# Optimization experiments

Measured on AMD Instinct MI355X. Metric: run time of the kernel, lower is better.

Reference implementation:

```python
import jax, jax.numpy as jnp
import numpy as np

B, T_OUT, C, L = 8, 8, 64, 1024  # batch, temporal channels, spatial channels (=in_channels), time steps


def setup_inputs() -> dict:
    key = jax.random.key(0)
    ks = jax.random.split(key, 7)
    s = 1.0 / np.sqrt(C)  # conv1d default init scale
    return {
        "x": jax.random.normal(ks[0], (B, T_OUT, C, L), dtype=jnp.float32),
        "Wq": jax.random.uniform(ks[1], (C, C), jnp.float32, -s, s),
        "bq": jax.random.uniform(ks[2], (C,), jnp.float32, -s, s),
        "Wk": jax.random.uniform(ks[3], (C, C), jnp.float32, -s, s),
        "bk": jax.random.uniform(ks[4], (C,), jnp.float32, -s, s),
        "Wv": jax.random.uniform(ks[5], (C, C), jnp.float32, -s, s),
        "bv": jax.random.uniform(ks[6], (C,), jnp.float32, -s, s),
    }


def reference(x, Wq, bq, Wk, bk, Wv, bv):
    b, t, c, l = x.shape
    xr = x.reshape(b * t, c, l)  # [BT, C, L]
    # 1x1 Conv1d == per-timestep linear over channels
    q = jnp.einsum('oc,bcl->bol', Wq, xr) + bq[:, None]
    k = jnp.einsum('oc,bcl->bol', Wk, xr) + bk[:, None]
    v = jnp.einsum('oc,bcl->bol', Wv, xr) + bv[:, None]
    # scores[b, i, j] = sum_c q[b, c, i] * k[b, c, j]  -> [BT, L, L]
    scores = jnp.einsum('bci,bcj->bij', q, k)
    weights = jax.nn.softmax(scores, axis=-1)
    # out[b, i, c] = sum_j weights[b, i, j] * v[b, c, j]
    out = jnp.einsum('bij,bcj->bic', weights, v)
    out = jnp.transpose(out, (0, 2, 1))  # [BT, C, L]
    return out.reshape(b, t, c, l)
```

## Files before the change

### kernel.cpp

```cpp
#include <hip/hip_runtime.h>
#include <hip/hip_bf16.h>

#define CC 64
#define LL 1024
#define LOG2E 1.44269504f

typedef unsigned short u16;
typedef unsigned int u32;
typedef __attribute__((ext_vector_type(8))) short short8;
typedef __attribute__((ext_vector_type(4))) float floatx4;

static __device__ __forceinline__ u16 f2b(float f) {
  return (u16)((__float_as_uint(f) + 0x8000u) >> 16);
}
static __device__ __forceinline__ u32 pk2(float a, float b) {
  return ((__float_as_uint(a) + 0x8000u) >> 16) |
         ((__float_as_uint(b) + 0x8000u) & 0xffff0000u);
}
static __device__ __forceinline__ u32 pk2t(float a, float b) {
  return __builtin_amdgcn_perm(__float_as_uint(b), __float_as_uint(a), 0x07060302u);
}
static __device__ __forceinline__ short8 mk8(u32 a, u32 b, u32 c, u32 d) {
  union { u32 u[4]; short8 s; } t;
  t.u[0] = a; t.u[1] = b; t.u[2] = c; t.u[3] = d;
  return t.s;
}

__global__ __launch_bounds__(256) void w_prep(
    const float* __restrict__ Wq, const float* __restrict__ bq,
    const float* __restrict__ Wk, const float* __restrict__ bk,
    const float* __restrict__ Wv, const float* __restrict__ bv,
    u16* __restrict__ whi, float* __restrict__ bsc)
{
  const int idx = blockIdx.x * 256 + threadIdx.x;
  const int m = idx >> 12;
  const float* W = (m == 0) ? Wq : (m == 1) ? Wk : Wv;
  const float w = W[idx & 4095] * ((m == 0) ? LOG2E : 1.0f);
  whi[idx] = f2b(w);
  if (blockIdx.x == 0 && threadIdx.x < 192)
    bsc[threadIdx.x] = (threadIdx.x < 64) ? bq[threadIdx.x] * LOG2E
                     : (threadIdx.x < 128) ? bk[threadIdx.x - 64] : bv[threadIdx.x - 128];
}

__global__ __launch_bounds__(256) void qkv_kernel(
    const float* __restrict__ x,
    const u16* __restrict__ whi, const float* __restrict__ bsc,
    u16* __restrict__ qT, u16* __restrict__ kT, u16* __restrict__ vO)
{
  __shared__ __align__(16) u16 xh_s[2][64 * 72];
  __shared__ __align__(16) u16 tbuf[4 * 16 * 72];
  __shared__ float b_s[192];

  const int tid  = threadIdx.x;
  const int wave = tid >> 6;
  const int lane = tid & 63;
  const int l16  = lane & 15;
  const int quad = lane >> 4;

  const int bt = blockIdx.x & 63;
  const int l0 = (blockIdx.x >> 6) << 7;

  const int lx = tid & 63;
  const int cg = (tid >> 6) << 4;
  const float* xp = x + ((size_t)bt * CC + cg) * LL + l0 + lx;

  {
    float v0[16];
    #pragma unroll
    for (int e = 0; e < 16; ++e) v0[e] = xp[(size_t)e * LL];
    #pragma unroll
    for (int e = 0; e < 16; e += 2)
      *(u32*)(&xh_s[0][0] + lx * 72 + cg + e) = pk2(v0[e], v0[e + 1]);
    if (tid < 192) b_s[tid] = bsc[tid];
  }
  __syncthreads();

  float v1[16];
  #pragma unroll
  for (int e = 0; e < 16; ++e) v1[e] = xp[64 + (size_t)e * LL];

  u16* tb = tbuf + wave * (16 * 72);

  auto compute = [&](int ch) {
    const int lc0 = l0 + (ch << 6);
    const u16* xr_h = &xh_s[ch][0] + (wave * 16 + l16) * 72 + quad * 8;
    const short8 xh0 = *(const short8*)(xr_h);
    const short8 xh1 = *(const short8*)(xr_h + 32);

    #pragma unroll
    for (int ot = 0; ot < 12; ++ot) {
      const int m = ot >> 2;
      const int off = (m << 12) + (((ot & 3) * 16 + l16) << 6) + quad * 8;
      const short8 ah0 = *(const short8*)(whi + off);
      const short8 ah1 = *(const short8*)(whi + off + 32);

      floatx4 acc = (floatx4){0.f, 0.f, 0.f, 0.f};
      acc = __builtin_amdgcn_mfma_f32_16x16x32_bf16(ah0, xh0, acc, 0, 0, 0);
      acc = __builtin_amdgcn_mfma_f32_16x16x32_bf16(ah1, xh1, acc, 0, 0, 0);

      float ov[4];
      #pragma unroll
      for (int r = 0; r < 4; ++r)
        ov[r] = acc[r] + b_s[ot * 16 + quad * 4 + r];

      if (ot < 8) {
        uint2 pv;
        pv.x = pk2(ov[0], ov[1]);
        pv.y = pk2(ov[2], ov[3]);
        *(uint2*)(tb + l16 * 72 + (ot & 3) * 16 + quad * 4) = pv;
        if ((ot & 3) == 3) {
          asm volatile("" ::: "memory");
          u16* gdst = ((ot < 4) ? qT : kT) + ((size_t)(bt * LL + lc0 + wave * 16)) * CC;
          const int rr = lane >> 3;
          const int c8 = (lane & 7) * 8;
          #pragma unroll
          for (int s2 = 0; s2 < 2; ++s2) {
            const int row = s2 * 8 + rr;
            uint4 val = *(const uint4*)(tb + row * 72 + c8);
            *(uint4*)(gdst + row * CC + c8) = val;
          }
          asm volatile("" ::: "memory");
        }
      } else {
        const int ob = (ot - 8) * 16 + quad * 4;
        u16* vdst = vO + ((size_t)(bt * CC + ob)) * LL + lc0 + wave * 16 + l16;
        #pragma unroll
        for (int r = 0; r < 4; ++r)
          vdst[(size_t)r * LL] = f2b(ov[r]);
      }
    }
  };

  compute(0);

  #pragma unroll
  for (int e = 0; e < 16; e += 2)
    *(u32*)(&xh_s[1][0] + lx * 72 + cg + e) = pk2(v1[e], v1[e + 1]);
  __syncthreads();

  compute(1);
}

__global__ __launch_bounds__(256) void attn_kernel(
    const u16* __restrict__ qT, const u16* __restrict__ kT,
    const u16* __restrict__ vB, float* __restrict__ out)
{
  __shared__ __align__(16) u16 smem[18432];
  const int tid  = threadIdx.x;
  const int wave = tid >> 6;
  const int lane = tid & 63;
  const int l16  = lane & 15;
  const int quad = lane >> 4;

  const int bt    = blockIdx.x & 63;
  const int chunk = blockIdx.x >> 6;
  const int i0w   = (chunk << 7) + (wave << 5);

  const u16* kbase = kT + (size_t)bt * LL * CC;
  const u16* vbase = vB + (size_t)bt * CC * LL;

  short8 qf[2][2];
  {
    const u16* qb = qT + (size_t)bt * LL * CC;
    #pragma unroll
    for (int s = 0; s < 2; ++s) {
      const u16* qr = qb + (size_t)(i0w + s * 16 + l16) * CC + quad * 8;
      qf[s][0] = *(const short8*)(qr);
      qf[s][1] = *(const short8*)(qr + 32);
    }
  }

  floatx4 O[2][4];
  #pragma unroll
  for (int s = 0; s < 2; ++s)
    #pragma unroll
    for (int cf = 0; cf < 4; ++cf)
      O[s][cf] = (floatx4){0.f, 0.f, 0.f, 0.f};
  float lsA[2] = {0.f, 0.f}, lsB[2] = {0.f, 0.f};

  const int r_st = tid >> 2;
  const int c_st = (tid & 3) << 4;
  const int sr = (r_st & 0x20) | ((r_st & 4) << 2) | ((r_st & 0x18) >> 1) | (r_st & 3);

  {
    uint4 k0 = *(const uint4*)(kbase + (size_t)r_st * CC + c_st);
    uint4 k1 = *(const uint4*)(kbase + (size_t)r_st * CC + c_st + 8);
    uint4 v0 = *(const uint4*)(vbase + (size_t)r_st * LL + c_st);
    uint4 v1 = *(const uint4*)(vbase + (size_t)r_st * LL + c_st + 8);
    *(uint4*)(smem + sr * 72 + c_st)              = k0;
    *(uint4*)(smem + sr * 72 + c_st + 8)          = k1;
    *(uint4*)(smem + 4608 + r_st * 72 + c_st)     = v0;
    *(uint4*)(smem + 4608 + r_st * 72 + c_st + 8) = v1;
  }
  __syncthreads();

  for (int it = 0; it < 16; ++it) {
    u16* ktc = smem + (it & 1) * 9216;
    u16* vtc = ktc + 4608;

    uint4 rk0, rk1, rv0, rv1;
    if (it < 15) {
      const int jb = (it + 1) << 6;
      rk0 = *(const uint4*)(kbase + (size_t)(jb + r_st) * CC + c_st);
      rk1 = *(const uint4*)(kbase + (size_t)(jb + r_st) * CC + c_st + 8);
      rv0 = *(const uint4*)(vbase + (size_t)r_st * LL + jb + c_st);
      rv1 = *(const uint4*)(vbase + (size_t)r_st * LL + jb + c_st + 8);
    }

    floatx4 S[2][4];
    #pragma unroll
    for (int jt = 0; jt < 4; ++jt) {
      const u16* ka = ktc + (jt * 16 + l16) * 72 + quad * 8;
      const short8 a0 = *(const short8*)(ka);
      const short8 a1 = *(const short8*)(ka + 32);
      #pragma unroll
      for (int s = 0; s < 2; ++s) {
        floatx4 acc = (floatx4){0.f, 0.f, 0.f, 0.f};
        acc = __builtin_amdgcn_mfma_f32_16x16x32_bf16(a0, qf[s][0], acc, 0, 0, 0);
        acc = __builtin_amdgcn_mfma_f32_16x16x32_bf16(a1, qf[s][1], acc, 0, 0, 0);
        S[s][jt] = acc;
      }
    }

    uint2 pp[2][4];
    #pragma unroll
    for (int s = 0; s < 2; ++s)
      #pragma unroll
      for (int jt = 0; jt < 4; ++jt) {
        const float e0 = __builtin_amdgcn_exp2f(S[s][jt][0]);
        const float e1 = __builtin_amdgcn_exp2f(S[s][jt][1]);
        const float e2 = __builtin_amdgcn_exp2f(S[s][jt][2]);
        const float e3 = __builtin_amdgcn_exp2f(S[s][jt][3]);
        lsA[s] += e0 + e1;
        lsB[s] += e2 + e3;
        pp[s][jt].x = pk2t(e0, e1);
        pp[s][jt].y = pk2t(e2, e3);
      }

    short8 v0f[4], v1f[4];
    #pragma unroll
    for (int cf = 0; cf < 4; ++cf) {
      const u16* va = vtc + (cf * 16 + l16) * 72 + quad * 8;
      v0f[cf] = *(const short8*)(va);
      v1f[cf] = *(const short8*)(va + 32);
    }

    #pragma unroll
    for (int s = 0; s < 2; ++s) {
      const short8 pa0 = mk8(pp[s][0].x, pp[s][0].y, pp[s][1].x, pp[s][1].y);
      const short8 pa1 = mk8(pp[s][2].x, pp[s][2].y, pp[s][3].x, pp[s][3].y);
      #pragma unroll
      for (int cf = 0; cf < 4; ++cf) {
        O[s][cf] = __builtin_amdgcn_mfma_f32_16x16x32_bf16(pa0, v0f[cf], O[s][cf], 0, 0, 0);
        O[s][cf] = __builtin_amdgcn_mfma_f32_16x16x32_bf16(pa1, v1f[cf], O[s][cf], 0, 0, 0);
      }
    }

    if (it < 15) {
      u16* ktn = smem + ((it + 1) & 1) * 9216;
      *(uint4*)(ktn + sr * 72 + c_st)              = rk0;
      *(uint4*)(ktn + sr * 72 + c_st + 8)          = rk1;
      *(uint4*)(ktn + 4608 + r_st * 72 + c_st)     = rv0;
      *(uint4*)(ktn + 4608 + r_st * 72 + c_st + 8) = rv1;
    }
    __syncthreads();
  }

  float lsum[2];
  #pragma unroll
  for (int s = 0; s < 2; ++s) {
    lsum[s] = lsA[s] + lsB[s];
    lsum[s] += __shfl_xor(lsum[s], 16, 64);
    lsum[s] += __shfl_xor(lsum[s], 32, 64);
  }

  __syncthreads();
  float* of = (float*)smem + wave * 1280;
  #pragma unroll
  for (int s = 0; s < 2; ++s) {
    #pragma unroll
    for (int r = 0; r < 4; ++r) {
      const float rl = __builtin_amdgcn_rcpf(__shfl(lsum[s], quad * 4 + r, 64));
      #pragma unroll
      for (int cf = 0; cf < 4; ++cf)
        O[s][cf][r] *= rl;
    }
    asm volatile("" ::: "memory");
    #pragma unroll
    for (int cf = 0; cf < 4; ++cf)
      #pragma unroll
      for (int r = 0; r < 4; ++r)
        of[(cf * 16 + l16) * 20 + quad * 4 + r] = O[s][cf][r];
    asm volatile("" ::: "memory");
    float* ob = out + ((size_t)bt * CC) * LL + i0w + s * 16;
    #pragma unroll
    for (int rr = 0; rr < 4; ++rr) {
      const int c = rr * 16 + l16;
      float4 val = *(const float4*)(of + c * 20 + quad * 4);
      *(float4*)(ob + (size_t)c * LL + quad * 4) = val;
    }
    asm volatile("" ::: "memory");
  }
}

extern "C" void kernel_launch(void* const* d_in, const int* in_sizes, int n_in,
                              void* d_out, int out_size, void* d_ws, size_t ws_size,
                              hipStream_t stream) {
  const float* x  = (const float*)d_in[0];
  const float* Wq = (const float*)d_in[1];
  const float* bq = (const float*)d_in[2];
  const float* Wk = (const float*)d_in[3];
  const float* bk = (const float*)d_in[4];
  const float* Wv = (const float*)d_in[5];
  const float* bv = (const float*)d_in[6];
  float* out = (float*)d_out;

  u16* qTp = (u16*)d_ws;
  u16* kTp = qTp + (size_t)64 * LL * CC;
  u16* vp  = kTp + (size_t)64 * LL * CC;
  u16* whi = vp  + (size_t)64 * LL * CC;
  float* bsc = (float*)(whi + 3 * 64 * 64);

  w_prep<<<48, 256, 0, stream>>>(Wq, bq, Wk, bk, Wv, bv, whi, bsc);
  qkv_kernel<<<512, 256, 0, stream>>>(x, whi, bsc, qTp, kTp, vp);
  attn_kernel<<<512, 256, 0, stream>>>(qTp, kTp, vp, out);
}
```

Measured before the change: 119.0 us.

## Fuse QKV projection and attention into one cooperative kernel with grid sync

Merges the weight-prep, QKV projection and attention kernels into a single cooperative launch with a grid-wide barrier between the phases. Each block now converts the weights to bf16 directly into shared memory instead of reading them from a separate prep kernel. Separately, it adds s_setprio around the MFMA sections and moves the V fragment loads ahead of the exp computation. The aim is to remove launch overhead and inter-kernel gaps, at the cost of redundant per-block weight conversion, a grid sync, and reliance on 512 blocks being co-resident; if the cooperative launch fails it falls back to two kernels.

```diff
diff --git a/kernel.cpp b/kernel.cpp
--- a/kernel.cpp
+++ b/kernel.cpp
@@ -1,5 +1,5 @@
 #include <hip/hip_runtime.h>
-#include <hip/hip_bf16.h>
+#include <hip/hip_cooperative_groups.h>
 
 #define CC 64
 #define LL 1024
@@ -26,30 +26,20 @@
   return t.s;
 }
 
-__global__ __launch_bounds__(256) void w_prep(
+#define LDS_U16 28032
+
+static __device__ __forceinline__ void qkv_body(
+    const float* __restrict__ x,
     const float* __restrict__ Wq, const float* __restrict__ bq,
     const float* __restrict__ Wk, const float* __restrict__ bk,
     const float* __restrict__ Wv, const float* __restrict__ bv,
-    u16* __restrict__ whi, float* __restrict__ bsc)
-{
-  const int idx = blockIdx.x * 256 + threadIdx.x;
-  const int m = idx >> 12;
-  const float* W = (m == 0) ? Wq : (m == 1) ? Wk : Wv;
-  const float w = W[idx & 4095] * ((m == 0) ? LOG2E : 1.0f);
-  whi[idx] = f2b(w);
-  if (blockIdx.x == 0 && threadIdx.x < 192)
-    bsc[threadIdx.x] = (threadIdx.x < 64) ? bq[threadIdx.x] * LOG2E
-                     : (threadIdx.x < 128) ? bk[threadIdx.x - 64] : bv[threadIdx.x - 128];
-}
-
-__global__ __launch_bounds__(256) void qkv_kernel(
-    const float* __restrict__ x,
-    const u16* __restrict__ whi, const float* __restrict__ bsc,
-    u16* __restrict__ qT, u16* __restrict__ kT, u16* __restrict__ vO)
-{
-  __shared__ __align__(16) u16 xh_s[2][64 * 72];
-  __shared__ __align__(16) u16 tbuf[4 * 16 * 72];
-  __shared__ float b_s[192];
+    u16* __restrict__ qT, u16* __restrict__ kT, u16* __restrict__ vO,
+    u16* smem_u)
+{
+  u16* const whi_s  = smem_u;
+  u16* const xh_s   = smem_u + 13824;
+  u16* const tbuf_s = smem_u + 23040;
+  float* const b_s  = (float*)(smem_u + 27648);
 
   const int tid  = threadIdx.x;
   const int wave = tid >> 6;
@@ -64,35 +54,48 @@
   const int cg = (tid >> 6) << 4;
   const float* xp = x + ((size_t)bt * CC + cg) * LL + l0 + lx;
 
-  {
-    float v0[16];
-    #pragma unroll
-    for (int e = 0; e < 16; ++e) v0[e] = xp[(size_t)e * LL];
-    #pragma unroll
-    for (int e = 0; e < 16; e += 2)
-      *(u32*)(&xh_s[0][0] + lx * 72 + cg + e) = pk2(v0[e], v0[e + 1]);
-    if (tid < 192) b_s[tid] = bsc[tid];
-  }
+  float v0[16];
+  #pragma unroll
+  for (int e = 0; e < 16; ++e) v0[e] = xp[(size_t)e * LL];
+
+  #pragma unroll
+  for (int rep = 0; rep < 24; ++rep) {
+    const int i = (rep * 256 + tid) * 2;
+    const int m = i >> 12;
+    const int r = (i >> 6) & 63;
+    const int c = i & 63;
+    const int j = i & 4095;
+    const float* W = (m == 0) ? Wq : (m == 1) ? Wk : Wv;
+    const float sc = (m == 0) ? LOG2E : 1.0f;
+    *(u32*)(whi_s + m * 4608 + r * 72 + c) = pk2(W[j] * sc, W[j + 1] * sc);
+  }
+  if (tid < 192)
+    b_s[tid] = (tid < 64) ? bq[tid] * LOG2E
+             : (tid < 128) ? bk[tid - 64] : bv[tid - 128];
+
+  #pragma unroll
+  for (int e = 0; e < 16; e += 2)
+    *(u32*)(xh_s + lx * 72 + cg + e) = pk2(v0[e], v0[e + 1]);
   __syncthreads();
 
   float v1[16];
   #pragma unroll
   for (int e = 0; e < 16; ++e) v1[e] = xp[64 + (size_t)e * LL];
 
-  u16* tb = tbuf + wave * (16 * 72);
+  u16* tb = tbuf_s + wave * 1152;
 
   auto compute = [&](int ch) {
     const int lc0 = l0 + (ch << 6);
-    const u16* xr_h = &xh_s[ch][0] + (wave * 16 + l16) * 72 + quad * 8;
+    const u16* xr_h = xh_s + ch * 4608 + (wave * 16 + l16) * 72 + quad * 8;
     const short8 xh0 = *(const short8*)(xr_h);
     const short8 xh1 = *(const short8*)(xr_h + 32);
 
     #pragma unroll
     for (int ot = 0; ot < 12; ++ot) {
       const int m = ot >> 2;
-      const int off = (m << 12) + (((ot & 3) * 16 + l16) << 6) + quad * 8;
-      const short8 ah0 = *(const short8*)(whi + off);
-      const short8 ah1 = *(const short8*)(whi + off + 32);
+      const int off = m * 4608 + ((ot & 3) * 16 + l16) * 72 + quad * 8;
+      const short8 ah0 = *(const short8*)(whi_s + off);
+      const short8 ah1 = *(const short8*)(whi_s + off + 32);
 
       floatx4 acc = (floatx4){0.f, 0.f, 0.f, 0.f};
       acc = __builtin_amdgcn_mfma_f32_16x16x32_bf16(ah0, xh0, acc, 0, 0, 0);
@@ -135,17 +138,17 @@
 
   #pragma unroll
   for (int e = 0; e < 16; e += 2)
-    *(u32*)(&xh_s[1][0] + lx * 72 + cg + e) = pk2(v1[e], v1[e + 1]);
+    *(u32*)(xh_s + 4608 + lx * 72 + cg + e) = pk2(v1[e], v1[e + 1]);
   __syncthreads();
 
   compute(1);
 }
 
-__global__ __launch_bounds__(256) void attn_kernel(
+static __device__ __forceinline__ void attn_body(
     const u16* __restrict__ qT, const u16* __restrict__ kT,
-    const u16* __restrict__ vB, float* __restrict__ out)
-{
-  __shared__ __align__(16) u16 smem[18432];
+    const u16* __restrict__ vB, float* __restrict__ out,
+    u16* smem)
+{
   const int tid  = threadIdx.x;
   const int wave = tid >> 6;
   const int lane = tid & 63;
@@ -208,6 +211,7 @@
     }
 
     floatx4 S[2][4];
+    __builtin_amdgcn_s_setprio(1);
     #pragma unroll
     for (int jt = 0; jt < 4; ++jt) {
       const u16* ka = ktc + (jt * 16 + l16) * 72 + quad * 8;
@@ -220,6 +224,15 @@
         acc = __builtin_amdgcn_mfma_f32_16x16x32_bf16(a1, qf[s][1], acc, 0, 0, 0);
         S[s][jt] = acc;
       }
+    }
+    __builtin_amdgcn_s_setprio(0);
+
+    short8 v0f[4], v1f[4];
+    #pragma unroll
+    for (int cf = 0; cf < 4; ++cf) {
+      const u16* va = vtc + (cf * 16 + l16) * 72 + quad * 8;
+      v0f[cf] = *(const short8*)(va);
+      v1f[cf] = *(const short8*)(va + 32);
     }
 
     uint2 pp[2][4];
@@ -237,14 +250,7 @@
         pp[s][jt].y = pk2t(e2, e3);
       }
 
-    short8 v0f[4], v1f[4];
-    #pragma unroll
-    for (int cf = 0; cf < 4; ++cf) {
-      const u16* va = vtc + (cf * 16 + l16) * 72 + quad * 8;
-      v0f[cf] = *(const short8*)(va);
-      v1f[cf] = *(const short8*)(va + 32);
-    }
-
+    __builtin_amdgcn_s_setprio(1);
     #pragma unroll
     for (int s = 0; s < 2; ++s) {
       const short8 pa0 = mk8(pp[s][0].x, pp[s][0].y, pp[s][1].x, pp[s][1].y);
@@ -255,6 +261,7 @@
         O[s][cf] = __builtin_amdgcn_mfma_f32_16x16x32_bf16(pa1, v1f[cf], O[s][cf], 0, 0, 0);
       }
     }
+    __builtin_amdgcn_s_setprio(0);
 
     if (it < 15) {
       u16* ktn = smem + ((it + 1) & 1) * 9216;
@@ -301,6 +308,39 @@
     }
     asm volatile("" ::: "memory");
   }
+}
+
+__global__ __launch_bounds__(256) void qkv_kernel(
+    const float* __restrict__ x,
+    const float* __restrict__ Wq, const float* __restrict__ bq,
+    const float* __restrict__ Wk, const float* __restrict__ bk,
+    const float* __restrict__ Wv, const float* __restrict__ bv,
+    u16* __restrict__ qT, u16* __restrict__ kT, u16* __restrict__ vO)
+{
+  __shared__ __align__(16) u16 s[LDS_U16];
+  qkv_body(x, Wq, bq, Wk, bk, Wv, bv, qT, kT, vO, s);
+}
+
+__global__ __launch_bounds__(256) void attn_kernel(
+    const u16* __restrict__ qT, const u16* __restrict__ kT,
+    const u16* __restrict__ vB, float* __restrict__ out)
+{
+  __shared__ __align__(16) u16 s[18432];
+  attn_body(qT, kT, vB, out, s);
+}
+
+__global__ __launch_bounds__(256, 2) void fused_kernel(
+    const float* __restrict__ x,
+    const float* __restrict__ Wq, const float* __restrict__ bq,
+    const float* __restrict__ Wk, const float* __restrict__ bk,
+    const float* __restrict__ Wv, const float* __restrict__ bv,
+    u16* __restrict__ qT, u16* __restrict__ kT, u16* __restrict__ vO,
+    float* __restrict__ out)
+{
+  __shared__ __align__(16) u16 s[LDS_U16];
+  qkv_body(x, Wq, bq, Wk, bk, Wv, bv, qT, kT, vO, s);
+  cooperative_groups::this_grid().sync();
+  attn_body(qT, kT, vO, out, s);
 }
 
 extern "C" void kernel_launch(void* const* d_in, const int* in_sizes, int n_in,
@@ -318,10 +358,14 @@
   u16* qTp = (u16*)d_ws;
   u16* kTp = qTp + (size_t)64 * LL * CC;
   u16* vp  = kTp + (size_t)64 * LL * CC;
-  u16* whi = vp  + (size_t)64 * LL * CC;
-  float* bsc = (float*)(whi + 3 * 64 * 64);
-
-  w_prep<<<48, 256, 0, stream>>>(Wq, bq, Wk, bk, Wv, bv, whi, bsc);
-  qkv_kernel<<<512, 256, 0, stream>>>(x, whi, bsc, qTp, kTp, vp);
-  attn_kernel<<<512, 256, 0, stream>>>(qTp, kTp, vp, out);
-}
+
+  void* args[] = {(void*)&x, (void*)&Wq, (void*)&bq, (void*)&Wk, (void*)&bk,
+                  (void*)&Wv, (void*)&bv, (void*)&qTp, (void*)&kTp, (void*)&vp,
+                  (void*)&out};
+  hipError_t e = hipLaunchCooperativeKernel((const void*)fused_kernel,
+                                            dim3(512), dim3(256), args, 0, stream);
+  if (e != hipSuccess) {
+    qkv_kernel<<<512, 256, 0, stream>>>(x, Wq, bq, Wk, bk, Wv, bv, qTp, kTp, vp);
+    attn_kernel<<<512, 256, 0, stream>>>(qTp, kTp, vp, out);
+  }
+}
```

Result: slower. 194.6 us (+63.5%).

## Drop LDS staging in QKV and attention; use single-wave attention blocks

Applied to the files above, without the earlier changes.

The attention kernel becomes one 64-thread wave per block over 2048 blocks. Each wave now reads K and V fragments straight from global memory (L2) instead of staging them in double-buffered shared memory behind a __syncthreads per tile. To make those direct reads line up, the QKV kernel writes K already row-permuted in global memory, matching the order the old shared-memory swizzle produced. It also loads x straight into registers without an LDS transpose and uses twice as many blocks, each covering half as many positions. The aim is to remove block barriers and LDS round trips and to raise scheduling flexibility, at the cost of redundant global/L2 traffic for K/V across waves and less data reuse.

```diff
diff --git a/kernel.cpp b/kernel.cpp
--- a/kernel.cpp
+++ b/kernel.cpp
@@ -1,5 +1,4 @@
 #include <hip/hip_runtime.h>
-#include <hip/hip_bf16.h>
 
 #define CC 64
 #define LL 1024
@@ -47,9 +46,7 @@
     const u16* __restrict__ whi, const float* __restrict__ bsc,
     u16* __restrict__ qT, u16* __restrict__ kT, u16* __restrict__ vO)
 {
-  __shared__ __align__(16) u16 xh_s[2][64 * 72];
-  __shared__ __align__(16) u16 tbuf[4 * 16 * 72];
-  __shared__ float b_s[192];
+  __shared__ __align__(16) u16 tbuf_s[4 * 16 * 72];
 
   const int tid  = threadIdx.x;
   const int wave = tid >> 6;
@@ -58,116 +55,101 @@
   const int quad = lane >> 4;
 
   const int bt = blockIdx.x & 63;
-  const int l0 = (blockIdx.x >> 6) << 7;
-
-  const int lx = tid & 63;
-  const int cg = (tid >> 6) << 4;
-  const float* xp = x + ((size_t)bt * CC + cg) * LL + l0 + lx;
-
-  {
-    float v0[16];
-    #pragma unroll
-    for (int e = 0; e < 16; ++e) v0[e] = xp[(size_t)e * LL];
-    #pragma unroll
-    for (int e = 0; e < 16; e += 2)
-      *(u32*)(&xh_s[0][0] + lx * 72 + cg + e) = pk2(v0[e], v0[e + 1]);
-    if (tid < 192) b_s[tid] = bsc[tid];
-  }
-  __syncthreads();
-
-  float v1[16];
-  #pragma unroll
-  for (int e = 0; e < 16; ++e) v1[e] = xp[64 + (size_t)e * LL];
-
-  u16* tb = tbuf + wave * (16 * 72);
-
-  auto compute = [&](int ch) {
-    const int lc0 = l0 + (ch << 6);
-    const u16* xr_h = &xh_s[ch][0] + (wave * 16 + l16) * 72 + quad * 8;
-    const short8 xh0 = *(const short8*)(xr_h);
-    const short8 xh1 = *(const short8*)(xr_h + 32);
-
-    #pragma unroll
-    for (int ot = 0; ot < 12; ++ot) {
-      const int m = ot >> 2;
-      const int off = (m << 12) + (((ot & 3) * 16 + l16) << 6) + quad * 8;
-      const short8 ah0 = *(const short8*)(whi + off);
-      const short8 ah1 = *(const short8*)(whi + off + 32);
-
-      floatx4 acc = (floatx4){0.f, 0.f, 0.f, 0.f};
-      acc = __builtin_amdgcn_mfma_f32_16x16x32_bf16(ah0, xh0, acc, 0, 0, 0);
-      acc = __builtin_amdgcn_mfma_f32_16x16x32_bf16(ah1, xh1, acc, 0, 0, 0);
-
-      float ov[4];
-      #pragma unroll
-      for (int r = 0; r < 4; ++r)
-        ov[r] = acc[r] + b_s[ot * 16 + quad * 4 + r];
-
-      if (ot < 8) {
-        uint2 pv;
-        pv.x = pk2(ov[0], ov[1]);
-        pv.y = pk2(ov[2], ov[3]);
-        *(uint2*)(tb + l16 * 72 + (ot & 3) * 16 + quad * 4) = pv;
-        if ((ot & 3) == 3) {
-          asm volatile("" ::: "memory");
-          u16* gdst = ((ot < 4) ? qT : kT) + ((size_t)(bt * LL + lc0 + wave * 16)) * CC;
-          const int rr = lane >> 3;
-          const int c8 = (lane & 7) * 8;
+  const int l0 = (blockIdx.x >> 6) << 6;
+  const int l  = l0 + wave * 16 + l16;
+
+  const float* xb = x + (size_t)bt * CC * LL + l;
+  float xv0[8], xv1[8];
+  #pragma unroll
+  for (int e = 0; e < 8; ++e) {
+    xv0[e] = xb[(size_t)(quad * 8 + e) * LL];
+    xv1[e] = xb[(size_t)(quad * 8 + 32 + e) * LL];
+  }
+  const short8 xh0 = mk8(pk2(xv0[0], xv0[1]), pk2(xv0[2], xv0[3]),
+                         pk2(xv0[4], xv0[5]), pk2(xv0[6], xv0[7]));
+  const short8 xh1 = mk8(pk2(xv1[0], xv1[1]), pk2(xv1[2], xv1[3]),
+                         pk2(xv1[4], xv1[5]), pk2(xv1[6], xv1[7]));
+
+  u16* tb = tbuf_s + wave * 1152;
+
+  #pragma unroll
+  for (int ot = 0; ot < 12; ++ot) {
+    const int m = ot >> 2;
+    const int off = (m << 12) + (((ot & 3) * 16 + l16) << 6) + quad * 8;
+    const short8 ah0 = *(const short8*)(whi + off);
+    const short8 ah1 = *(const short8*)(whi + off + 32);
+
+    floatx4 acc = (floatx4){0.f, 0.f, 0.f, 0.f};
+    acc = __builtin_amdgcn_mfma_f32_16x16x32_bf16(ah0, xh0, acc, 0, 0, 0);
+    acc = __builtin_amdgcn_mfma_f32_16x16x32_bf16(ah1, xh1, acc, 0, 0, 0);
+
+    const float4 bb = *(const float4*)(bsc + ot * 16 + quad * 4);
+    float ov[4];
+    ov[0] = acc[0] + bb.x; ov[1] = acc[1] + bb.y;
+    ov[2] = acc[2] + bb.z; ov[3] = acc[3] + bb.w;
+
+    if (ot < 8) {
+      uint2 pv;
+      pv.x = pk2(ov[0], ov[1]);
+      pv.y = pk2(ov[2], ov[3]);
+      *(uint2*)(tb + l16 * 72 + (ot & 3) * 16 + quad * 4) = pv;
+      if ((ot & 3) == 3) {
+        asm volatile("" ::: "memory");
+        const int rr = lane >> 3;
+        const int c8 = (lane & 7) * 8;
+        if (ot < 4) {
+          u16* gdst = qT + ((size_t)(bt * LL + l0 + wave * 16)) * CC;
           #pragma unroll
           for (int s2 = 0; s2 < 2; ++s2) {
             const int row = s2 * 8 + rr;
             uint4 val = *(const uint4*)(tb + row * 72 + c8);
             *(uint4*)(gdst + row * CC + c8) = val;
           }
-          asm volatile("" ::: "memory");
+        } else {
+          u16* gdst = kT + ((size_t)(bt * LL + l0 + (wave >> 1) * 32)) * CC;
+          #pragma unroll
+          for (int s2 = 0; s2 < 2; ++s2) {
+            const int row = s2 * 8 + rr;
+            const int q2 = (wave & 1) * 2 + s2;
+            const int srow = ((rr >> 2) << 4) + (q2 << 2) + (rr & 3);
+            uint4 val = *(const uint4*)(tb + row * 72 + c8);
+            *(uint4*)(gdst + srow * CC + c8) = val;
+          }
         }
-      } else {
-        const int ob = (ot - 8) * 16 + quad * 4;
-        u16* vdst = vO + ((size_t)(bt * CC + ob)) * LL + lc0 + wave * 16 + l16;
-        #pragma unroll
-        for (int r = 0; r < 4; ++r)
-          vdst[(size_t)r * LL] = f2b(ov[r]);
-      }
-    }
-  };
-
-  compute(0);
-
-  #pragma unroll
-  for (int e = 0; e < 16; e += 2)
-    *(u32*)(&xh_s[1][0] + lx * 72 + cg + e) = pk2(v1[e], v1[e + 1]);
-  __syncthreads();
-
-  compute(1);
-}
-
-__global__ __launch_bounds__(256) void attn_kernel(
+        asm volatile("" ::: "memory");
+      }
+    } else {
+      const int ob = (ot - 8) * 16 + quad * 4;
+      u16* vdst = vO + ((size_t)(bt * CC + ob)) * LL + l0 + wave * 16 + l16;
+      #pragma unroll
+      for (int r = 0; r < 4; ++r)
+        vdst[(size_t)r * LL] = f2b(ov[r]);
+    }
+  }
+}
+
+__global__ __launch_bounds__(64) void attn_kernel(
     const u16* __restrict__ qT, const u16* __restrict__ kT,
     const u16* __restrict__ vB, float* __restrict__ out)
 {
-  __shared__ __align__(16) u16 smem[18432];
-  const int tid  = threadIdx.x;
-  const int wave = tid >> 6;
-  const int lane = tid & 63;
+  __shared__ __align__(16) float of_s[1280];
+  const int lane = threadIdx.x;
   const int l16  = lane & 15;
   const int quad = lane >> 4;
 
   const int bt    = blockIdx.x & 63;
   const int chunk = blockIdx.x >> 6;
-  const int i0w   = (chunk << 7) + (wave << 5);
+  const int i0    = chunk << 5;
 
   const u16* kbase = kT + (size_t)bt * LL * CC;
   const u16* vbase = vB + (size_t)bt * CC * LL;
 
   short8 qf[2][2];
-  {
-    const u16* qb = qT + (size_t)bt * LL * CC;
-    #pragma unroll
-    for (int s = 0; s < 2; ++s) {
-      const u16* qr = qb + (size_t)(i0w + s * 16 + l16) * CC + quad * 8;
-      qf[s][0] = *(const short8*)(qr);
-      qf[s][1] = *(const short8*)(qr + 32);
-    }
+  #pragma unroll
+  for (int s = 0; s < 2; ++s) {
+    const u16* qr = qT + (size_t)bt * LL * CC + (size_t)(i0 + s * 16 + l16) * CC + quad * 8;
+    qf[s][0] = *(const short8*)(qr);
+    qf[s][1] = *(const short8*)(qr + 32);
   }
 
   floatx4 O[2][4];
@@ -176,41 +158,23 @@
     #pragma unroll
     for (int cf = 0; cf < 4; ++cf)
       O[s][cf] = (floatx4){0.f, 0.f, 0.f, 0.f};
-  float lsA[2] = {0.f, 0.f}, lsB[2] = {0.f, 0.f};
-
-  const int r_st = tid >> 2;
-  const int c_st = (tid & 3) << 4;
-  const int sr = (r_st & 0x20) | ((r_st & 4) << 2) | ((r_st & 0x18) >> 1) | (r_st & 3);
-
-  {
-    uint4 k0 = *(const uint4*)(kbase + (size_t)r_st * CC + c_st);
-    uint4 k1 = *(const uint4*)(kbase + (size_t)r_st * CC + c_st + 8);
-    uint4 v0 = *(const uint4*)(vbase + (size_t)r_st * LL + c_st);
-    uint4 v1 = *(const uint4*)(vbase + (size_t)r_st * LL + c_st + 8);
-    *(uint4*)(smem + sr * 72 + c_st)              = k0;
-    *(uint4*)(smem + sr * 72 + c_st + 8)          = k1;
-    *(uint4*)(smem + 4608 + r_st * 72 + c_st)     = v0;
-    *(uint4*)(smem + 4608 + r_st * 72 + c_st + 8) = v1;
-  }
-  __syncthreads();
+  float ls[2] = {0.f, 0.f};
 
   for (int it = 0; it < 16; ++it) {
-    u16* ktc = smem + (it & 1) * 9216;
-    u16* vtc = ktc + 4608;
-
-    uint4 rk0, rk1, rv0, rv1;
-    if (it < 15) {
-      const int jb = (it + 1) << 6;
-      rk0 = *(const uint4*)(kbase + (size_t)(jb + r_st) * CC + c_st);
-      rk1 = *(const uint4*)(kbase + (size_t)(jb + r_st) * CC + c_st + 8);
-      rv0 = *(const uint4*)(vbase + (size_t)r_st * LL + jb + c_st);
-      rv1 = *(const uint4*)(vbase + (size_t)r_st * LL + jb + c_st + 8);
-    }
+    const int jb = it << 6;
+
+    uint4 vf[2][4];
+    #pragma unroll
+    for (int p = 0; p < 2; ++p)
+      #pragma unroll
+      for (int cf = 0; cf < 4; ++cf)
+        vf[p][cf] = *(const uint4*)(vbase + (size_t)(cf * 16 + l16) * LL
+                                    + jb + p * 32 + quad * 8);
 
     floatx4 S[2][4];
     #pragma unroll
     for (int jt = 0; jt < 4; ++jt) {
-      const u16* ka = ktc + (jt * 16 + l16) * 72 + quad * 8;
+      const u16* ka = kbase + (size_t)(jb + jt * 16 + l16) * CC + quad * 8;
       const short8 a0 = *(const short8*)(ka);
       const short8 a1 = *(const short8*)(ka + 32);
       #pragma unroll
@@ -231,19 +195,10 @@
         const float e1 = __builtin_amdgcn_exp2f(S[s][jt][1]);
         const float e2 = __builtin_amdgcn_exp2f(S[s][jt][2]);
         const float e3 = __builtin_amdgcn_exp2f(S[s][jt][3]);
-        lsA[s] += e0 + e1;
-        lsB[s] += e2 + e3;
+        ls[s] += (e0 + e1) + (e2 + e3);
         pp[s][jt].x = pk2t(e0, e1);
         pp[s][jt].y = pk2t(e2, e3);
       }
-
-    short8 v0f[4], v1f[4];
-    #pragma unroll
-    for (int cf = 0; cf < 4; ++cf) {
-      const u16* va = vtc + (cf * 16 + l16) * 72 + quad * 8;
-      v0f[cf] = *(const short8*)(va);
-      v1f[cf] = *(const short8*)(va + 32);
-    }
 
     #pragma unroll
     for (int s = 0; s < 2; ++s) {
@@ -251,36 +206,25 @@
       const short8 pa1 = mk8(pp[s][2].x, pp[s][2].y, pp[s][3].x, pp[s][3].y);
       #pragma unroll
       for (int cf = 0; cf < 4; ++cf) {
-        O[s][cf] = __builtin_amdgcn_mfma_f32_16x16x32_bf16(pa0, v0f[cf], O[s][cf], 0, 0, 0);
-        O[s][cf] = __builtin_amdgcn_mfma_f32_16x16x32_bf16(pa1, v1f[cf], O[s][cf], 0, 0, 0);
-      }
-    }
-
-    if (it < 15) {
-      u16* ktn = smem + ((it + 1) & 1) * 9216;
-      *(uint4*)(ktn + sr * 72 + c_st)              = rk0;
-      *(uint4*)(ktn + sr * 72 + c_st + 8)          = rk1;
-      *(uint4*)(ktn + 4608 + r_st * 72 + c_st)     = rv0;
-      *(uint4*)(ktn + 4608 + r_st * 72 + c_st + 8) = rv1;
-    }
-    __syncthreads();
-  }
-
-  float lsum[2];
+        const short8 vb0 = mk8(vf[0][cf].x, vf[0][cf].y, vf[0][cf].z, vf[0][cf].w);
+        const short8 vb1 = mk8(vf[1][cf].x, vf[1][cf].y, vf[1][cf].z, vf[1][cf].w);
+        O[s][cf] = __builtin_amdgcn_mfma_f32_16x16x32_bf16(pa0, vb0, O[s][cf], 0, 0, 0);
+        O[s][cf] = __builtin_amdgcn_mfma_f32_16x16x32_bf16(pa1, vb1, O[s][cf], 0, 0, 0);
+      }
+    }
+  }
+
   #pragma unroll
   for (int s = 0; s < 2; ++s) {
-    lsum[s] = lsA[s] + lsB[s];
-    lsum[s] += __shfl_xor(lsum[s], 16, 64);
-    lsum[s] += __shfl_xor(lsum[s], 32, 64);
-  }
-
-  __syncthreads();
-  float* of = (float*)smem + wave * 1280;
+    ls[s] += __shfl_xor(ls[s], 16, 64);
+    ls[s] += __shfl_xor(ls[s], 32, 64);
+  }
+
   #pragma unroll
   for (int s = 0; s < 2; ++s) {
     #pragma unroll
     for (int r = 0; r < 4; ++r) {
-      const float rl = __builtin_amdgcn_rcpf(__shfl(lsum[s], quad * 4 + r, 64));
+      const float rl = __builtin_amdgcn_rcpf(__shfl(ls[s], quad * 4 + r, 64));
       #pragma unroll
       for (int cf = 0; cf < 4; ++cf)
         O[s][cf][r] *= rl;
@@ -290,14 +234,16 @@
     for (int cf = 0; cf < 4; ++cf)
       #pragma unroll
       for (int r = 0; r < 4; ++r)
-        of[(cf * 16 + l16) * 20 + quad * 4 + r] = O[s][cf][r];
+        of_s[(cf * 16 + l16) * 20 + quad * 4 + r] = O[s][cf][r];
     asm volatile("" ::: "memory");
-    float* ob = out + ((size_t)bt * CC) * LL + i0w + s * 16;
-    #pragma unroll
-    for (int rr = 0; rr < 4; ++rr) {
-      const int c = rr * 16 + l16;
-      float4 val = *(const float4*)(of + c * 20 + quad * 4);
-      *(float4*)(ob + (size_t)c * LL + quad * 4) = val;
+    {
+      float* ob = out + (size_t)bt * CC * LL + i0 + s * 16;
+      #pragma unroll
+      for (int rr = 0; rr < 4; ++rr) {
+        const int c = rr * 16 + l16;
+        float4 val = *(const float4*)(of_s + c * 20 + quad * 4);
+        *(float4*)(ob + (size_t)c * LL + quad * 4) = val;
+      }
     }
     asm volatile("" ::: "memory");
   }
@@ -322,6 +268,6 @@
   float* bsc = (float*)(whi + 3 * 64 * 64);
 
   w_prep<<<48, 256, 0, stream>>>(Wq, bq, Wk, bk, Wv, bv, whi, bsc);
-  qkv_kernel<<<512, 256, 0, stream>>>(x, whi, bsc, qTp, kTp, vp);
-  attn_kernel<<<512, 256, 0, stream>>>(qTp, kTp, vp, out);
-}
+  qkv_kernel<<<1024, 256, 0, stream>>>(x, whi, bsc, qTp, kTp, vp);
+  attn_kernel<<<2048, 64, 0, stream>>>(qTp, kTp, vp, out);
+}
```

New measurement: 156.9 us. +31.8%, slower.
